# Kernel optimization log

Measured on AMD Instinct MI355X. Metric: run time of the kernel, lower is better.

The kernel has to match this reference:

```python
import jax, jax.numpy as jnp
import numpy as np

EMBED_DIM = 1024
N_TOKENS = 8192


def setup_inputs() -> dict:
    key = jax.random.key(0)
    kx, kr, ke = jax.random.split(key, 3)
    x = jax.random.normal(kx, (N_TOKENS, EMBED_DIM), dtype=jnp.float32)
    rotation_params = jax.random.normal(kr, (EMBED_DIM * EMBED_DIM,), dtype=jnp.float32) * 0.02
    entangle_params = jax.random.normal(ke, (EMBED_DIM * EMBED_DIM,), dtype=jnp.float32) * 0.02
    return {"x": x, "rotation_params": rotation_params, "entangle_params": entangle_params}


def reference(x, rotation_params, entangle_params):
    d = EMBED_DIM
    w_q = rotation_params.reshape(d, d)
    w_k = entangle_params.reshape(d, d)
    q = x @ w_q                      # [N, D]
    k = x @ w_k                      # [N, D]
    v = x                            # v is the raw input (as in source)
    scale = 1.0 / np.sqrt(d).astype(np.float32)
    scores = jax.nn.softmax(jnp.einsum('nd,md->nm', q, k) * scale, axis=-1)  # [N, N]
    return scores @ v                # [N, D]
```

## Files before the change

### kernel.cpp

```cpp
#include <hip/hip_runtime.h>
#include <hip/hip_bf16.h>
#include <stdint.h>

#define EMBED 1024
#define NTOK 8192
#define QRANGE 4.5f

#define BUFB (48 * 1024)
#define SMEM_TOTAL (3 * BUFB)

typedef short bf16x8 __attribute__((ext_vector_type(8)));
typedef float f32x4 __attribute__((ext_vector_type(4)));
typedef int int4v __attribute__((ext_vector_type(4)));

__device__ inline unsigned short f2bf(float f) {
    union { float f; unsigned u; } c; c.f = f;
    unsigned u = c.u;
    unsigned r = (u + 0x7fffu + ((u >> 16) & 1u)) >> 16;
    return (unsigned short)r;
}

__device__ __forceinline__ void bar_sync_drain() {
    asm volatile("s_waitcnt vmcnt(0)\n\ts_barrier" ::: "memory");
}
__device__ __forceinline__ void bar_sync_cnt6() {
    asm volatile("s_waitcnt vmcnt(6)\n\ts_barrier" ::: "memory");
}

__device__ inline void xcd_remap(int& bx, int& by) {
    if ((gridDim.y & 7) == 0) {
        int bid = by * gridDim.x + bx;
        by = bid % gridDim.y;
        bx = bid / gridDim.y;
    }
}

__global__ void prep_x(const float* __restrict__ x, unsigned short* __restrict__ xb,
                       unsigned short* __restrict__ xbT) {
    __shared__ unsigned short tile[32][33];
    int bj = blockIdx.x, bi = blockIdx.y;
    int tx = threadIdx.x, ty = threadIdx.y;
#pragma unroll
    for (int r = 0; r < 4; ++r) {
        int row = ty + r * 8;
        size_t gi = (size_t)(bi * 32 + row) * EMBED + bj * 32 + tx;
        unsigned short h = f2bf(x[gi]);
        xb[gi] = h;
        tile[row][tx] = h;
    }
    __syncthreads();
#pragma unroll
    for (int r = 0; r < 4; ++r) {
        int row = ty + r * 8;
        xbT[(size_t)(bj * 32 + row) * NTOK + bi * 32 + tx] = tile[tx][row];
    }
}

__global__ void prep_w2(const float* __restrict__ wq, const float* __restrict__ wk,
                        unsigned short* __restrict__ wT, float* __restrict__ Z) {
    if (blockIdx.z == 2) {
        if (blockIdx.x == 0 && blockIdx.y == 0) {
            int t = threadIdx.y * 32 + threadIdx.x;
            for (int i = t; i < NTOK; i += 256) Z[i] = 0.f;
        }
        return;
    }
    __shared__ unsigned short tile[32][33];
    int bj = blockIdx.x, bi = blockIdx.y;
    int tx = threadIdx.x, ty = threadIdx.y;
    const float* w = blockIdx.z ? wk : wq;
    unsigned short* dst = wT + (size_t)blockIdx.z * EMBED * EMBED;
#pragma unroll
    for (int r = 0; r < 4; ++r) {
        int row = ty + r * 8;
        tile[row][tx] = f2bf(w[(size_t)(bi * 32 + row) * EMBED + bj * 32 + tx]);
    }
    __syncthreads();
#pragma unroll
    for (int r = 0; r < 4; ++r) {
        int row = ty + r * 8;
        dst[(size_t)(bj * 32 + row) * EMBED + bi * 32 + tx] = tile[tx][row];
    }
}

template<int MODE> struct GAcc { using T = f32x4; };
template<> struct GAcc<1> { using T = int4v; };
template<int MODE> struct GFrag { using T = bf16x8; };
template<> struct GFrag<1> { using T = int4v; };

__device__ __forceinline__ void stage256(const char* __restrict__ A,
                                         const char* __restrict__ B,
                                         char* dst, size_t aBase, size_t bBase,
                                         int ldA, int ldB, int kB, int tid) {
    const int srow = tid >> 3;
    const int csw  = ((tid & 7) ^ (srow & 7)) << 4;
    const int dof  = srow * 128 + ((tid & 7) << 4);
    const char* ga = A + (aBase + srow) * (size_t)ldA + kB + csw;
    const char* gb = B + (bBase + srow) * (size_t)ldB + kB + csw;
    char* da = dst + dof;
    char* db = dst + 32768 + dof;
#pragma unroll
    for (int it = 0; it < 4; ++it)
        __builtin_amdgcn_global_load_lds(
            (const __attribute__((address_space(1))) void*)(ga + (size_t)it * 64 * ldA),
            (__attribute__((address_space(3))) void*)(da + it * 64 * 128), 16, 0, 0);
#pragma unroll
    for (int it = 0; it < 2; ++it)
        __builtin_amdgcn_global_load_lds(
            (const __attribute__((address_space(1))) void*)(gb + (size_t)it * 64 * ldB),
            (__attribute__((address_space(3))) void*)(db + it * 64 * 128), 16, 0, 0);
}

template<int MODE>
__device__ __forceinline__ void ld_frags(typename GFrag<MODE>::T (&af)[4],
                                         typename GFrag<MODE>::T (&bf)[4],
                                         const char* As, const char* Bs,
                                         int wm, int wn, int l15, int quad, int s) {
    using FT = typename GFrag<MODE>::T;
    const int sl = ((((s << 2) + quad) ^ (l15 & 7)) << 4);
#pragma unroll
    for (int f = 0; f < 4; ++f) {
        af[f] = *(const FT*)(As + (wm + f * 16 + l15) * 128 + sl);
        bf[f] = *(const FT*)(Bs + (wn + f * 16 + l15) * 128 + sl);
    }
}

template<int MODE>
__device__ __forceinline__ void mfma16(typename GAcc<MODE>::T (&acc)[4][4],
                                       typename GFrag<MODE>::T (&af)[4],
                                       typename GFrag<MODE>::T (&bf)[4]) {
#pragma unroll
    for (int mt = 0; mt < 4; ++mt)
#pragma unroll
        for (int nt = 0; nt < 4; ++nt) {
            if constexpr (MODE == 1)
                acc[mt][nt] = __builtin_amdgcn_mfma_i32_16x16x64_i8(
                    af[mt], bf[nt], acc[mt][nt], 0, 0, 0);
            else
                acc[mt][nt] = __builtin_amdgcn_mfma_f32_16x16x32_bf16(
                    af[mt], bf[nt], acc[mt][nt], 0, 0, 0);
        }
}

template<int MODE>
__global__ __launch_bounds__(512, 2) void gemm256(
    const char* __restrict__ A, const char* __restrict__ B, void* __restrict__ Cv,
    int KB, int ldA, int ldB, int ldC, float qsc,
    float* __restrict__ Z, int beta, const float* __restrict__ Zn)
{
    extern __shared__ char smem[];
    const int tid  = threadIdx.x;
    const int lane = tid & 63;
    const int wid  = tid >> 6;
    const int wm   = (wid >> 1) << 6;
    const int wn   = (wid & 1) << 6;
    const int quad = lane >> 4;
    const int l15  = lane & 15;

    int bx = blockIdx.x, by = blockIdx.y;
    xcd_remap(bx, by);
    const size_t mBase = (size_t)by * 256;
    const size_t nBase = (size_t)bx * 128;

    using FT = typename GFrag<MODE>::T;
    typename GAcc<MODE>::T acc[4][4] = {};
    FT a0[4], b0[4], a1[4], b1[4];

    const int nsteps = KB >> 7;
    stage256(A, B, smem, mBase, nBase, ldA, ldB, 0, tid);
    if (nsteps > 1) {
        stage256(A, B, smem + BUFB, mBase, nBase, ldA, ldB, 128, tid);
        bar_sync_cnt6();
    } else {
        bar_sync_drain();
    }
    __builtin_amdgcn_sched_barrier(0);
    ld_frags<MODE>(a0, b0, smem, smem + 32768, wm, wn, l15, quad, 0);

    int bc = 0;
    for (int t = 0; t < nsteps; ++t) {
        const char* As = smem + bc * BUFB;
        ld_frags<MODE>(a1, b1, As, As + 32768, wm, wn, l15, quad, 1);
        __builtin_amdgcn_s_setprio(1);
        mfma16<MODE>(acc, a0, b0);
        __builtin_amdgcn_s_setprio(0);
        if (t + 1 < nsteps) {
            bar_sync_drain();
            __builtin_amdgcn_sched_barrier(0);
            int bn = bc + 1; if (bn >= 3) bn -= 3;
            const char* An = smem + bn * BUFB;
            ld_frags<MODE>(a0, b0, An, An + 32768, wm, wn, l15, quad, 0);
            if (t + 2 < nsteps) {
                int bs = bc + 2; if (bs >= 3) bs -= 3;
                stage256(A, B, smem + bs * BUFB, mBase, nBase, ldA, ldB,
                         (t + 2) << 7, tid);
            }
        }
        __builtin_amdgcn_s_setprio(1);
        mfma16<MODE>(acc, a1, b1);
        __builtin_amdgcn_s_setprio(0);
        ++bc; if (bc >= 3) bc -= 3;
    }
    __syncthreads();

    if constexpr (MODE == 0) {
        float* stf = (float*)smem + wid * (16 * 68);
        unsigned char* C = (unsigned char*)Cv;
        const float qinv = 127.0f / QRANGE;
#pragma unroll
        for (int mt = 0; mt < 4; ++mt) {
#pragma unroll
            for (int nt = 0; nt < 4; ++nt) {
                f32x4 v = acc[mt][nt];
#pragma unroll
                for (int r = 0; r < 4; ++r)
                    stf[(quad * 4 + r) * 68 + nt * 16 + l15] = v[r];
            }
#pragma unroll
            for (int pass = 0; pass < 4; ++pass) {
                int row = pass * 4 + (lane >> 4);
                int cc  = (lane & 15) * 4;
                f32x4 vv = *(const f32x4*)(stf + row * 68 + cc);
                int b[4];
#pragma unroll
                for (int r = 0; r < 4; ++r)
                    b[r] = __float2int_rn(fminf(fmaxf(vv[r] * qinv, -127.f), 127.f));
                int pk = (b[0] & 0xff) | ((b[1] & 0xff) << 8) |
                         ((b[2] & 0xff) << 16) | (b[3] << 24);
                size_t grow = mBase + wm + mt * 16 + row;
                *(int*)(C + grow * (size_t)ldC + nBase + wn + cc) = pk;
            }
        }
    } else if constexpr (MODE == 2) {
        float* stf = (float*)smem + wid * (16 * 68);
        float* C = (float*)Cv;
#pragma unroll
        for (int mt = 0; mt < 4; ++mt) {
#pragma unroll
            for (int nt = 0; nt < 4; ++nt) {
                f32x4 v = acc[mt][nt];
#pragma unroll
                for (int r = 0; r < 4; ++r)
                    stf[(quad * 4 + r) * 68 + nt * 16 + l15] = v[r];
            }
#pragma unroll
            for (int pass = 0; pass < 4; ++pass) {
                int row = pass * 4 + (lane >> 4);
                int cc  = (lane & 15) * 4;
                f32x4 vv = *(const f32x4*)(stf + row * 68 + cc);
                size_t grow = mBase + wm + mt * 16 + row;
                float* gp = C + grow * (size_t)ldC + nBase + wn + cc;
                if (beta) {
                    f32x4 old = *(const f32x4*)gp;
                    vv = vv + old;
                }
                if (Zn) {
                    float inv = 1.0f / Zn[grow];
                    vv = vv * inv;
                }
                *(f32x4*)gp = vv;
            }
        }
    } else {
        unsigned short* st = (unsigned short*)smem + wid * (16 * 72);
        unsigned short* C = (unsigned short*)Cv;
#pragma unroll
        for (int mt = 0; mt < 4; ++mt) {
            float rs[4] = {0.f, 0.f, 0.f, 0.f};
#pragma unroll
            for (int nt = 0; nt < 4; ++nt) {
                int4v v = acc[mt][nt];
#pragma unroll
                for (int r = 0; r < 4; ++r) {
                    float e = __expf((float)v[r] * qsc);
                    rs[r] += e;
                    st[(quad * 4 + r) * 72 + nt * 16 + l15] = f2bf(e);
                }
            }
#pragma unroll
            for (int r = 0; r < 4; ++r) {
                float s = rs[r];
                s += __shfl_xor(s, 1);
                s += __shfl_xor(s, 2);
                s += __shfl_xor(s, 4);
                s += __shfl_xor(s, 8);
                if (l15 == 0)
                    atomicAdd(&Z[mBase + wm + mt * 16 + quad * 4 + r], s);
            }
#pragma unroll
            for (int pass = 0; pass < 2; ++pass) {
                int row = pass * 8 + (lane >> 3);
                int cc  = (lane & 7) * 8;
                bf16x8 vv = *(const bf16x8*)(st + row * 72 + cc);
                size_t grow = mBase + wm + mt * 16 + row;
                *(bf16x8*)(C + grow * (size_t)ldC + nBase + wn + cc) = vv;
            }
        }
    }
}

extern "C" void kernel_launch(void* const* d_in, const int* in_sizes, int n_in,
                              void* d_out, int out_size, void* d_ws, size_t ws_size,
                              hipStream_t stream) {
    const float* x  = (const float*)d_in[0];
    const float* wq = (const float*)d_in[1];
    const float* wk = (const float*)d_in[2];
    float* out = (float*)d_out;

    char* p = (char*)d_ws;
    unsigned short* xb   = (unsigned short*)p; p += (size_t)NTOK * EMBED * 2;
    unsigned short* xbT  = (unsigned short*)p; p += (size_t)NTOK * EMBED * 2;
    signed char*    qk8  = (signed char*)p;    p += (size_t)NTOK * 2 * EMBED;
    unsigned short* wqkT = (unsigned short*)p; p += (size_t)2 * EMBED * EMBED * 2;
    float* Z = (float*)p; p += (size_t)NTOK * 4;
    unsigned short* P = (unsigned short*)p;

    size_t used  = (size_t)(p - (char*)d_ws);
    size_t avail = ws_size > used ? (ws_size - used) / 2 : 0;
    int NC = NTOK;
    while (NC > 128 && (size_t)NTOK * NC > avail) NC >>= 1;

    hipFuncSetAttribute((const void*)gemm256<0>,
                        hipFuncAttributeMaxDynamicSharedMemorySize, SMEM_TOTAL);
    hipFuncSetAttribute((const void*)gemm256<1>,
                        hipFuncAttributeMaxDynamicSharedMemorySize, SMEM_TOTAL);
    hipFuncSetAttribute((const void*)gemm256<2>,
                        hipFuncAttributeMaxDynamicSharedMemorySize, SMEM_TOTAL);

    prep_x<<<dim3(EMBED / 32, NTOK / 32), dim3(32, 8), 0, stream>>>(x, xb, xbT);
    prep_w2<<<dim3(32, 32, 3), dim3(32, 8), 0, stream>>>(wq, wk, wqkT, Z);

    gemm256<0><<<dim3(2 * EMBED / 128, NTOK / 256), 512, SMEM_TOTAL, stream>>>(
        (const char*)xb, (const char*)wqkT, qk8,
        2 * EMBED, 2 * EMBED, 2 * EMBED, 2 * EMBED,
        0.f, nullptr, 0, nullptr);

    const char* q8 = (const char*)qk8;
    const char* k8 = q8 + EMBED;
    const float qsc = (QRANGE / 127.0f) * (QRANGE / 127.0f) / 32.0f;
    for (int c0 = 0; c0 < NTOK; c0 += NC) {
        const bool last = (c0 + NC >= NTOK);
        gemm256<1><<<dim3(NC / 128, NTOK / 256), 512, SMEM_TOTAL, stream>>>(
            q8, k8 + (size_t)c0 * 2 * EMBED, P,
            EMBED, 2 * EMBED, 2 * EMBED, NC,
            qsc, Z, 0, nullptr);
        gemm256<2><<<dim3(EMBED / 128, NTOK / 256), 512, SMEM_TOTAL, stream>>>(
            (const char*)P, (const char*)(xbT + c0), out,
            NC * 2, NC * 2, NTOK * 2, EMBED,
            0.f, nullptr, c0 > 0 ? 1 : 0, last ? Z : nullptr);
    }
}
```

Baseline: 341.2 us.

## Use 256x256 tiles with double buffering for projection and score GEMMs

```diff
diff --git a/kernel.cpp b/kernel.cpp
--- a/kernel.cpp
+++ b/kernel.cpp
@@ -8,6 +8,8 @@
 
 #define BUFB (48 * 1024)
 #define SMEM_TOTAL (3 * BUFB)
+#define BBUF (64 * 1024)
+#define SMEM_BIG (2 * BBUF)
 
 typedef short bf16x8 __attribute__((ext_vector_type(8)));
 typedef float f32x4 __attribute__((ext_vector_type(4)));
@@ -88,51 +90,55 @@
 template<int MODE> struct GFrag { using T = bf16x8; };
 template<> struct GFrag<1> { using T = int4v; };
 
+__device__ __forceinline__ void stage_rows(const char* __restrict__ G, char* dst,
+                                           size_t base, int ld, int kB, int tid,
+                                           int niter) {
+    const int srow = tid >> 3;
+    const int csw  = ((tid & 7) ^ (srow & 7)) << 4;
+    const int dof  = srow * 128 + ((tid & 7) << 4);
+    const char* g = G + (base + srow) * (size_t)ld + kB + csw;
+    char* d = dst + dof;
+    for (int it = 0; it < niter; ++it)
+        __builtin_amdgcn_global_load_lds(
+            (const __attribute__((address_space(1))) void*)(g + (size_t)it * 64 * ld),
+            (__attribute__((address_space(3))) void*)(d + it * 64 * 128), 16, 0, 0);
+}
+
 __device__ __forceinline__ void stage256(const char* __restrict__ A,
                                          const char* __restrict__ B,
                                          char* dst, size_t aBase, size_t bBase,
                                          int ldA, int ldB, int kB, int tid) {
-    const int srow = tid >> 3;
-    const int csw  = ((tid & 7) ^ (srow & 7)) << 4;
-    const int dof  = srow * 128 + ((tid & 7) << 4);
-    const char* ga = A + (aBase + srow) * (size_t)ldA + kB + csw;
-    const char* gb = B + (bBase + srow) * (size_t)ldB + kB + csw;
-    char* da = dst + dof;
-    char* db = dst + 32768 + dof;
-#pragma unroll
-    for (int it = 0; it < 4; ++it)
-        __builtin_amdgcn_global_load_lds(
-            (const __attribute__((address_space(1))) void*)(ga + (size_t)it * 64 * ldA),
-            (__attribute__((address_space(3))) void*)(da + it * 64 * 128), 16, 0, 0);
-#pragma unroll
-    for (int it = 0; it < 2; ++it)
-        __builtin_amdgcn_global_load_lds(
-            (const __attribute__((address_space(1))) void*)(gb + (size_t)it * 64 * ldB),
-            (__attribute__((address_space(3))) void*)(db + it * 64 * 128), 16, 0, 0);
-}
-
-template<int MODE>
-__device__ __forceinline__ void ld_frags(typename GFrag<MODE>::T (&af)[4],
-                                         typename GFrag<MODE>::T (&bf)[4],
-                                         const char* As, const char* Bs,
-                                         int wm, int wn, int l15, int quad, int s) {
+    stage_rows(A, dst, aBase, ldA, kB, tid, 4);
+    stage_rows(B, dst + 32768, bBase, ldB, kB, tid, 2);
+}
+
+__device__ __forceinline__ void stage_big(const char* __restrict__ A,
+                                          const char* __restrict__ B,
+                                          char* dst, size_t aBase, size_t bBase,
+                                          int ldA, int ldB, int kB, int tid) {
+    stage_rows(A, dst, aBase, ldA, kB, tid, 4);
+    stage_rows(B, dst + 32768, bBase, ldB, kB, tid, 4);
+}
+
+template<int MODE, int NF>
+__device__ __forceinline__ void ld_fr(typename GFrag<MODE>::T (&fr)[NF],
+                                      const char* S, int wbase, int l15, int quad,
+                                      int s) {
     using FT = typename GFrag<MODE>::T;
     const int sl = ((((s << 2) + quad) ^ (l15 & 7)) << 4);
 #pragma unroll
-    for (int f = 0; f < 4; ++f) {
-        af[f] = *(const FT*)(As + (wm + f * 16 + l15) * 128 + sl);
-        bf[f] = *(const FT*)(Bs + (wn + f * 16 + l15) * 128 + sl);
-    }
-}
-
-template<int MODE>
-__device__ __forceinline__ void mfma16(typename GAcc<MODE>::T (&acc)[4][4],
-                                       typename GFrag<MODE>::T (&af)[4],
-                                       typename GFrag<MODE>::T (&bf)[4]) {
-#pragma unroll
-    for (int mt = 0; mt < 4; ++mt)
-#pragma unroll
-        for (int nt = 0; nt < 4; ++nt) {
+    for (int f = 0; f < NF; ++f)
+        fr[f] = *(const FT*)(S + (wbase + f * 16 + l15) * 128 + sl);
+}
+
+template<int MODE, int MT, int NT>
+__device__ __forceinline__ void mfma_mn(typename GAcc<MODE>::T (&acc)[MT][NT],
+                                        typename GFrag<MODE>::T (&af)[MT],
+                                        typename GFrag<MODE>::T (&bf)[NT]) {
+#pragma unroll
+    for (int mt = 0; mt < MT; ++mt)
+#pragma unroll
+        for (int nt = 0; nt < NT; ++nt) {
             if constexpr (MODE == 1)
                 acc[mt][nt] = __builtin_amdgcn_mfma_i32_16x16x64_i8(
                     af[mt], bf[nt], acc[mt][nt], 0, 0, 0);
@@ -175,21 +181,24 @@
         bar_sync_drain();
     }
     __builtin_amdgcn_sched_barrier(0);
-    ld_frags<MODE>(a0, b0, smem, smem + 32768, wm, wn, l15, quad, 0);
+    ld_fr<MODE, 4>(a0, smem, wm, l15, quad, 0);
+    ld_fr<MODE, 4>(b0, smem + 32768, wn, l15, quad, 0);
 
     int bc = 0;
     for (int t = 0; t < nsteps; ++t) {
         const char* As = smem + bc * BUFB;
-        ld_frags<MODE>(a1, b1, As, As + 32768, wm, wn, l15, quad, 1);
+        ld_fr<MODE, 4>(a1, As, wm, l15, quad, 1);
+        ld_fr<MODE, 4>(b1, As + 32768, wn, l15, quad, 1);
         __builtin_amdgcn_s_setprio(1);
-        mfma16<MODE>(acc, a0, b0);
+        mfma_mn<MODE, 4, 4>(acc, a0, b0);
         __builtin_amdgcn_s_setprio(0);
         if (t + 1 < nsteps) {
             bar_sync_drain();
             __builtin_amdgcn_sched_barrier(0);
             int bn = bc + 1; if (bn >= 3) bn -= 3;
             const char* An = smem + bn * BUFB;
-            ld_frags<MODE>(a0, b0, An, An + 32768, wm, wn, l15, quad, 0);
+            ld_fr<MODE, 4>(a0, An, wm, l15, quad, 0);
+            ld_fr<MODE, 4>(b0, An + 32768, wn, l15, quad, 0);
             if (t + 2 < nsteps) {
                 int bs = bc + 2; if (bs >= 3) bs -= 3;
                 stage256(A, B, smem + bs * BUFB, mBase, nBase, ldA, ldB,
@@ -197,41 +206,13 @@
             }
         }
         __builtin_amdgcn_s_setprio(1);
-        mfma16<MODE>(acc, a1, b1);
+        mfma_mn<MODE, 4, 4>(acc, a1, b1);
         __builtin_amdgcn_s_setprio(0);
         ++bc; if (bc >= 3) bc -= 3;
     }
     __syncthreads();
 
-    if constexpr (MODE == 0) {
-        float* stf = (float*)smem + wid * (16 * 68);
-        unsigned char* C = (unsigned char*)Cv;
-        const float qinv = 127.0f / QRANGE;
-#pragma unroll
-        for (int mt = 0; mt < 4; ++mt) {
-#pragma unroll
-            for (int nt = 0; nt < 4; ++nt) {
-                f32x4 v = acc[mt][nt];
-#pragma unroll
-                for (int r = 0; r < 4; ++r)
-                    stf[(quad * 4 + r) * 68 + nt * 16 + l15] = v[r];
-            }
-#pragma unroll
-            for (int pass = 0; pass < 4; ++pass) {
-                int row = pass * 4 + (lane >> 4);
-                int cc  = (lane & 15) * 4;
-                f32x4 vv = *(const f32x4*)(stf + row * 68 + cc);
-                int b[4];
-#pragma unroll
-                for (int r = 0; r < 4; ++r)
-                    b[r] = __float2int_rn(fminf(fmaxf(vv[r] * qinv, -127.f), 127.f));
-                int pk = (b[0] & 0xff) | ((b[1] & 0xff) << 8) |
-                         ((b[2] & 0xff) << 16) | (b[3] << 24);
-                size_t grow = mBase + wm + mt * 16 + row;
-                *(int*)(C + grow * (size_t)ldC + nBase + wn + cc) = pk;
-            }
-        }
-    } else if constexpr (MODE == 2) {
+    if constexpr (MODE == 2) {
         float* stf = (float*)smem + wid * (16 * 68);
         float* C = (float*)Cv;
 #pragma unroll
@@ -261,11 +242,87 @@
                 *(f32x4*)gp = vv;
             }
         }
+    }
+}
+
+template<int MODE>
+__global__ __launch_bounds__(512, 2) void gemmBig(
+    const char* __restrict__ A, const char* __restrict__ B, void* __restrict__ Cv,
+    int KB, int ldA, int ldB, int ldC, float qsc, float* __restrict__ Z)
+{
+    extern __shared__ char smem[];
+    const int tid  = threadIdx.x;
+    const int lane = tid & 63;
+    const int wid  = tid >> 6;
+    const int wm   = (wid >> 2) << 7;
+    const int wn   = (wid & 3) << 6;
+    const int quad = lane >> 4;
+    const int l15  = lane & 15;
+
+    int bx = blockIdx.x, by = blockIdx.y;
+    xcd_remap(bx, by);
+    const size_t mBase = (size_t)by * 256;
+    const size_t nBase = (size_t)bx * 256;
+
+    using FT = typename GFrag<MODE>::T;
+    typename GAcc<MODE>::T acc[8][4] = {};
+    FT af[8], bf[4];
+
+    const int nsteps = KB >> 7;
+    stage_big(A, B, smem, mBase, nBase, ldA, ldB, 0, tid);
+
+    for (int t = 0; t < nsteps; ++t) {
+        bar_sync_drain();
+        __builtin_amdgcn_sched_barrier(0);
+        if (t + 1 < nsteps)
+            stage_big(A, B, smem + ((t + 1) & 1) * BBUF, mBase, nBase, ldA, ldB,
+                      (t + 1) << 7, tid);
+        const char* As = smem + (t & 1) * BBUF;
+        const char* Bs = As + 32768;
+#pragma unroll
+        for (int s = 0; s < 2; ++s) {
+            ld_fr<MODE, 8>(af, As, wm, l15, quad, s);
+            ld_fr<MODE, 4>(bf, Bs, wn, l15, quad, s);
+            __builtin_amdgcn_s_setprio(1);
+            mfma_mn<MODE, 8, 4>(acc, af, bf);
+            __builtin_amdgcn_s_setprio(0);
+        }
+    }
+    __syncthreads();
+
+    if constexpr (MODE == 0) {
+        float* stf = (float*)smem + wid * (16 * 68);
+        unsigned char* C = (unsigned char*)Cv;
+        const float qinv = 127.0f / QRANGE;
+#pragma unroll
+        for (int mt = 0; mt < 8; ++mt) {
+#pragma unroll
+            for (int nt = 0; nt < 4; ++nt) {
+                f32x4 v = acc[mt][nt];
+#pragma unroll
+                for (int r = 0; r < 4; ++r)
+                    stf[(quad * 4 + r) * 68 + nt * 16 + l15] = v[r];
+            }
+#pragma unroll
+            for (int pass = 0; pass < 4; ++pass) {
+                int row = pass * 4 + (lane >> 4);
+                int cc  = (lane & 15) * 4;
+                f32x4 vv = *(const f32x4*)(stf + row * 68 + cc);
+                int b[4];
+#pragma unroll
+                for (int r = 0; r < 4; ++r)
+                    b[r] = __float2int_rn(fminf(fmaxf(vv[r] * qinv, -127.f), 127.f));
+                int pk = (b[0] & 0xff) | ((b[1] & 0xff) << 8) |
+                         ((b[2] & 0xff) << 16) | (b[3] << 24);
+                size_t grow = mBase + wm + mt * 16 + row;
+                *(int*)(C + grow * (size_t)ldC + nBase + wn + cc) = pk;
+            }
+        }
     } else {
         unsigned short* st = (unsigned short*)smem + wid * (16 * 72);
         unsigned short* C = (unsigned short*)Cv;
 #pragma unroll
-        for (int mt = 0; mt < 4; ++mt) {
+        for (int mt = 0; mt < 8; ++mt) {
             float rs[4] = {0.f, 0.f, 0.f, 0.f};
 #pragma unroll
             for (int nt = 0; nt < 4; ++nt) {
@@ -318,32 +375,32 @@
     size_t used  = (size_t)(p - (char*)d_ws);
     size_t avail = ws_size > used ? (ws_size - used) / 2 : 0;
     int NC = NTOK;
-    while (NC > 128 && (size_t)NTOK * NC > avail) NC >>= 1;
-
-    hipFuncSetAttribute((const void*)gemm256<0>,
-                        hipFuncAttributeMaxDynamicSharedMemorySize, SMEM_TOTAL);
-    hipFuncSetAttribute((const void*)gemm256<1>,
-                        hipFuncAttributeMaxDynamicSharedMemorySize, SMEM_TOTAL);
+    while (NC > 256 && (size_t)NTOK * NC > avail) NC >>= 1;
+
     hipFuncSetAttribute((const void*)gemm256<2>,
                         hipFuncAttributeMaxDynamicSharedMemorySize, SMEM_TOTAL);
+    hipFuncSetAttribute((const void*)gemmBig<0>,
+                        hipFuncAttributeMaxDynamicSharedMemorySize, SMEM_BIG);
+    hipFuncSetAttribute((const void*)gemmBig<1>,
+                        hipFuncAttributeMaxDynamicSharedMemorySize, SMEM_BIG);
 
     prep_x<<<dim3(EMBED / 32, NTOK / 32), dim3(32, 8), 0, stream>>>(x, xb, xbT);
     prep_w2<<<dim3(32, 32, 3), dim3(32, 8), 0, stream>>>(wq, wk, wqkT, Z);
 
-    gemm256<0><<<dim3(2 * EMBED / 128, NTOK / 256), 512, SMEM_TOTAL, stream>>>(
+    gemmBig<0><<<dim3(2 * EMBED / 256, NTOK / 256), 512, SMEM_BIG, stream>>>(
         (const char*)xb, (const char*)wqkT, qk8,
         2 * EMBED, 2 * EMBED, 2 * EMBED, 2 * EMBED,
-        0.f, nullptr, 0, nullptr);
+        0.f, nullptr);
 
     const char* q8 = (const char*)qk8;
     const char* k8 = q8 + EMBED;
     const float qsc = (QRANGE / 127.0f) * (QRANGE / 127.0f) / 32.0f;
     for (int c0 = 0; c0 < NTOK; c0 += NC) {
         const bool last = (c0 + NC >= NTOK);
-        gemm256<1><<<dim3(NC / 128, NTOK / 256), 512, SMEM_TOTAL, stream>>>(
+        gemmBig<1><<<dim3(NC / 256, NTOK / 256), 512, SMEM_BIG, stream>>>(
             q8, k8 + (size_t)c0 * 2 * EMBED, P,
             EMBED, 2 * EMBED, 2 * EMBED, NC,
-            qsc, Z, 0, nullptr);
+            qsc, Z);
         gemm256<2><<<dim3(EMBED / 128, NTOK / 256), 512, SMEM_TOTAL, stream>>>(
             (const char*)P, (const char*)(xbT + c0), out,
             NC * 2, NC * 2, NTOK * 2, EMBED,
```

Result: no change. 338.0 us (-0.9%).
